# Kernel tuning notes

Measured on AMD Instinct MI355X. Metric: run time of the kernel, lower is better.

The kernel has to match this reference:

```python
import jax, jax.numpy as jnp
import numpy as np

B, T, H, W, C = 2, 8, 60, 60, 256
HEADS = 8
HD = C // HEADS
WH, WW = 5, 6
SH, SW = 2, 3
N = WH * WW            # 30 tokens per window
NW = (H // WH) * (W // WW)  # 120 windows
HID = 4 * C
SCALE = HD ** -0.5


def _rel_pos_index():
    # standard Swin 2D relative position index, shape (N, N)
    coords = np.stack(np.meshgrid(np.arange(WH), np.arange(WW), indexing='ij')).reshape(2, -1)
    rel = (coords[:, :, None] - coords[:, None, :]).transpose(1, 2, 0).astype(np.int64)
    rel[..., 0] += WH - 1
    rel[..., 1] += WW - 1
    rel[..., 0] *= 2 * WW - 1
    return jnp.asarray(rel.sum(-1))


def _attn_mask():
    # shifted-window attention mask, shape (NW, N, N), values in {0, -100}
    img = np.zeros((H, W))
    cnt = 0
    for hs in (slice(0, -WH), slice(-WH, -SH), slice(-SH, None)):
        for ws in (slice(0, -WW), slice(-WW, -SW), slice(-SW, None)):
            img[hs, ws] = cnt
            cnt += 1
    mw = img.reshape(H // WH, WH, W // WW, WW).transpose(0, 2, 1, 3).reshape(NW, N)
    diff = mw[:, None, :] - mw[:, :, None]
    return jnp.asarray(np.where(diff != 0, -100.0, 0.0).astype(np.float32))


REL_INDEX = _rel_pos_index()
ATTN_MASK = _attn_mask()


def _ln(x, g, b):
    m = x.mean(-1, keepdims=True)
    v = ((x - m) ** 2).mean(-1, keepdims=True)
    return (x - m) / jnp.sqrt(v + 1e-5) * g + b


def setup_inputs() -> dict:
    key = jax.random.key(0)
    ks = jax.random.split(key, 8)
    w_scale = 0.02
    return {
        'x': jax.random.normal(ks[0], (B, T, H, W, C), jnp.float32),
        'contrast_embed': jax.random.normal(ks[1], (B, T, C), jnp.float32),
        'gamma1': jnp.ones((C,), jnp.float32),
        'beta1': jnp.zeros((C,), jnp.float32),
        'Wq': jax.random.normal(ks[2], (C, C), jnp.float32) * w_scale,
        'bq': jnp.zeros((C,), jnp.float32),
        'Wk': jax.random.normal(ks[3], (C, C), jnp.float32) * w_scale,
        'bk': jnp.zeros((C,), jnp.float32),
        'Wv': jax.random.normal(ks[4], (C, C), jnp.float32) * w_scale,
        'bv': jnp.zeros((C,), jnp.float32),
        'rel_bias': jax.random.normal(ks[5], ((2 * WH - 1) * (2 * WW - 1), HEADS), jnp.float32) * w_scale,
        'Wo': jax.random.normal(ks[6], (C, C), jnp.float32) * w_scale,
        'bo': jnp.zeros((C,), jnp.float32),
        'gamma2': jnp.ones((C,), jnp.float32),
        'beta2': jnp.zeros((C,), jnp.float32),
        'W1': jax.random.normal(ks[7], (C, HID), jnp.float32) * w_scale,
        'b1': jnp.zeros((HID,), jnp.float32),
        'W2': jax.random.normal(jax.random.fold_in(key, 99), (HID, C), jnp.float32) * w_scale,
        'b2': jnp.zeros((C,), jnp.float32),
    }


def reference(x, contrast_embed, gamma1, beta1, Wq, bq, Wk, bk, Wv, bv, rel_bias,
              Wo, bo, gamma2, beta2, W1, b1, W2, b2):
    shortcut = x
    xn = _ln(x, gamma1, beta1)
    # cyclic shift (SW-MSA)
    xs = jnp.roll(xn, (-SH, -SW), axis=(2, 3))
    # window partition: (B,T,H,W,C) -> (B*NW, T, N, C)
    w = xs.reshape(B, T, H // WH, WH, W // WW, WW, C)
    w = w.transpose(0, 2, 4, 1, 3, 5, 6).reshape(B * NW, T, N, C)
    # per-contrast positional embedding, broadcast over windows and spatial positions
    pos = jnp.broadcast_to(contrast_embed[:, None, :, None, :], (B, NW, T, 1, C)).reshape(B * NW, T, 1, C)
    wqk = w + pos
    q = (wqk @ Wq + bq).reshape(B * NW, T, N, HEADS, HD)
    k = (wqk @ Wk + bk).reshape(B * NW, T, N, HEADS, HD)
    v = (w @ Wv + bv).reshape(B * NW, T, N, HEADS, HD)
    scores = jnp.einsum('btnhd,btmhd->bthnm', q, k) * SCALE
    bias = rel_bias[REL_INDEX].transpose(2, 0, 1)  # (HEADS, N, N)
    scores = scores + bias
    scores = scores.reshape(B, NW, T, HEADS, N, N) + ATTN_MASK[None, :, None, None]
    attn = jax.nn.softmax(scores, axis=-1).reshape(B * NW, T, HEADS, N, N)
    out = jnp.einsum('bthnm,btmhd->btnhd', attn, v).reshape(B * NW, T, N, C)
    out = out @ Wo + bo
    # window reverse: (B*NW, T, N, C) -> (B, T, H, W, C)
    out = out.reshape(B, H // WH, W // WW, T, WH, WW, C)
    out = out.transpose(0, 3, 1, 4, 2, 5, 6).reshape(B, T, H, W, C)
    out = jnp.roll(out, (SH, SW), axis=(2, 3))
    x1 = shortcut + out
    h = jax.nn.gelu(_ln(x1, gamma2, beta2) @ W1 + b1, approximate=False) @ W2 + b2
    return x1 + h
```

## Files before the change

kernel.cpp:

```cpp
#include <hip/hip_runtime.h>

#define DI __device__ __forceinline__

constexpr int SH_=2, SW_=3;
constexpr int ROWS_=57600;
constexpr float SCALE_=0.17677669529663687f;

typedef unsigned short u16x8 __attribute__((ext_vector_type(8)));
typedef short bf16x8 __attribute__((ext_vector_type(8)));
typedef float f32x4 __attribute__((ext_vector_type(4)));
typedef float f32x16 __attribute__((ext_vector_type(16)));

DI float bf2f(unsigned short u){ return __uint_as_float(((unsigned int)u)<<16); }
DI unsigned short f2bf(float f){
  unsigned int u = __float_as_uint(f);
  u += 0x7fffu + ((u>>16)&1u);
  return (unsigned short)(u>>16);
}
DI float ldf(const void* p, size_t i, int f){
  return f ? ((const float*)p)[i] : bf2f(((const unsigned short*)p)[i]);
}
DI float4 ldf4(const void* p, size_t i, int f){
  if (f) return *((const float4*)((const float*)p + i));
  ushort4 u = *((const ushort4*)((const unsigned short*)p + i));
  return make_float4(bf2f(u.x),bf2f(u.y),bf2f(u.z),bf2f(u.w));
}

DI void gload16(const void* g, void* l){
  __builtin_amdgcn_global_load_lds((const __attribute__((address_space(1))) unsigned int*)g,
                                   (__attribute__((address_space(3))) unsigned int*)l, 16, 0, 0);
}

DI void xcd_remap(int wg, int nb, int nn, int& mt, int& nt){
  const int q = nb>>3, r = nb&7;
  const int x = wg & 7, i = wg >> 3;
  const int base = (x<r) ? x*(q+1) : r*(q+1) + (x-r)*q;
  const int work = base + i;
  mt = work / nn; nt = work - mt*nn;
}

#define WAITV(n) asm volatile("s_waitcnt vmcnt(" #n ")" ::: "memory")

__global__ void k_detect(const unsigned short* __restrict__ xu, int* __restrict__ flag){
  unsigned short u = xu[threadIdx.x*2];
  int insane = ((u>>7)&0xFF) > 0xC0;
  unsigned long long m = __ballot(insane);
  if (threadIdx.x==0) *flag = m ? 1 : 0;
}

__global__ __launch_bounds__(256) void k_prepw(
    const void* __restrict__ Wq, const void* __restrict__ Wk,
    const void* __restrict__ Wv, const void* __restrict__ Wo,
    const void* __restrict__ W1, const void* __restrict__ W2,
    unsigned short* __restrict__ wt, const int* __restrict__ flagp)
{
  const int f = *flagp;
  const void* src; int kb, total; size_t off;
  switch(blockIdx.y){
    case 0: src=Wq; kb=8;  total=65536;  off=0;      break;
    case 1: src=Wk; kb=8;  total=65536;  off=65536;  break;
    case 2: src=Wv; kb=8;  total=65536;  off=131072; break;
    case 3: src=Wo; kb=8;  total=65536;  off=196608; break;
    case 4: src=W1; kb=8;  total=262144; off=262144; break;
    default:src=W2; kb=10; total=262144; off=524288; break;
  }
  const int i = blockIdx.x*256 + threadIdx.x;
  if (i >= total) return;
  const int K = 1<<kb, N = total>>kb;
  const int n = i>>kb, k = i&(K-1);
  wt[off + (size_t)n*K + k] = f2bf(ldf(src, (size_t)k*N + n, f));
}

__global__ __launch_bounds__(256) void k_posqk(const void* __restrict__ ce,
    const unsigned short* __restrict__ wtq, const unsigned short* __restrict__ wtk,
    const void* __restrict__ bq, const void* __restrict__ bk,
    float* __restrict__ posq, float* __restrict__ posk, const int* __restrict__ flagp)
{
  const int f = *flagp;
  const int bt = blockIdx.x, mat = blockIdx.y, co = threadIdx.x;
  __shared__ float ces[256];
  ces[co] = ldf(ce, bt*256+co, f);
  __syncthreads();
  const unsigned short* wr = (mat ? wtk : wtq) + (size_t)co*256;
  float s = ldf(mat ? bk : bq, co, f);
  #pragma unroll
  for (int k0=0;k0<256;k0+=8){
    u16x8 wv = *(const u16x8*)(wr + k0);
    #pragma unroll
    for (int j=0;j<8;++j) s += ces[k0+j]*bf2f(wv[j]);
  }
  (mat ? posk : posq)[bt*256+co] = s;
}

__global__ __launch_bounds__(256) void k_ln1(const void* __restrict__ x,
    const void* __restrict__ g, const void* __restrict__ be,
    unsigned short* __restrict__ xw, const int* __restrict__ flagp)
{
  const int f = *flagp;
  const int lane = threadIdx.x & 63;
  const int wv   = threadIdx.x >> 6;
  const int rs   = blockIdx.x*4 + wv;
  float4 u = ldf4(x, (size_t)rs*256 + lane*4, f);
  float s = u.x+u.y+u.z+u.w;
  #pragma unroll
  for (int o=32;o;o>>=1) s += __shfl_xor(s,o,64);
  const float mean = s*(1.f/256.f);
  float d0=u.x-mean, d1=u.y-mean, d2=u.z-mean, d3=u.w-mean;
  float qv = d0*d0+d1*d1+d2*d2+d3*d3;
  #pragma unroll
  for (int o=32;o;o>>=1) qv += __shfl_xor(qv,o,64);
  const float rstd = rsqrtf(qv*(1.f/256.f)+1e-5f);
  float4 gu = ldf4(g, lane*4, f);
  float4 bu = ldf4(be, lane*4, f);
  ushort4 o;
  o.x = f2bf(d0*rstd*gu.x+bu.x);
  o.y = f2bf(d1*rstd*gu.y+bu.y);
  o.z = f2bf(d2*rstd*gu.z+bu.z);
  o.w = f2bf(d3*rstd*gu.w+bu.w);
  const int c = rs % 60, r = (rs/60)%60, t = (rs/3600)&7, b = rs/28800;
  int r2 = r - SH_; if (r2<0) r2+=60;
  int c2 = c - SW_; if (c2<0) c2+=60;
  const int a=r2/5, ii=r2%5, bb=c2/6, jj=c2%6;
  const int rw = ((b*120 + a*10+bb)*8 + t)*30 + ii*6+jj;
  *reinterpret_cast<ushort4*>(xw + (size_t)rw*256 + lane*4) = o;
}

__global__ __launch_bounds__(256) void k_ln2(const unsigned short* __restrict__ x1b,
    const void* __restrict__ g, const void* __restrict__ be,
    unsigned short* __restrict__ xn2, const int* __restrict__ flagp)
{
  const int f = *flagp;
  const int lane = threadIdx.x & 63;
  const int wv   = threadIdx.x >> 6;
  const int rs   = blockIdx.x*4 + wv;
  float4 v = ldf4(x1b, (size_t)rs*256 + lane*4, 0);
  float s = v.x+v.y+v.z+v.w;
  #pragma unroll
  for (int o=32;o;o>>=1) s += __shfl_xor(s,o,64);
  const float mean = s*(1.f/256.f);
  float d0=v.x-mean, d1=v.y-mean, d2=v.z-mean, d3=v.w-mean;
  float qv = d0*d0+d1*d1+d2*d2+d3*d3;
  #pragma unroll
  for (int o=32;o;o>>=1) qv += __shfl_xor(qv,o,64);
  const float rstd = rsqrtf(qv*(1.f/256.f)+1e-5f);
  float4 gu = ldf4(g, lane*4, f);
  float4 bu = ldf4(be, lane*4, f);
  ushort4 o;
  o.x = f2bf(d0*rstd*gu.x+bu.x);
  o.y = f2bf(d1*rstd*gu.y+bu.y);
  o.z = f2bf(d2*rstd*gu.z+bu.z);
  o.w = f2bf(d3*rstd*gu.w+bu.w);
  *reinterpret_cast<ushort4*>(xn2 + (size_t)rs*256 + lane*4) = o;
}

template<int K>
DI void mfma_core128(const unsigned short* __restrict__ A, const unsigned short* __restrict__ WT,
                     const int m0, const int n0, f32x4 acc[4][2], unsigned short* lds)
{
  constexpr int STEPS = K/32;
  const int tid = threadIdx.x, lane = tid&63, wave = tid>>6;
  const int wm = (wave>>2)*64, wn = (wave&3)*32;
  const int fr = lane&15;
  const int kqs = ((lane>>4) ^ ((fr>>1)&3))*8;
  #pragma unroll
  for (int i=0;i<4;++i)
    #pragma unroll
    for (int j=0;j<2;++j) acc[i][j] = (f32x4){0.f,0.f,0.f,0.f};
  const int isB = wave>>2;
  const int c0 = (wave&3)*128 + lane;
  const int c1 = c0 + 64;
  const int r0=c0>>2, p0=((c0&3)^((r0>>1)&3));
  const int r1=c1>>2, p1=((c1&3)^((r1>>1)&3));
  const unsigned short* gb = isB ? (WT + (size_t)n0*K) : (A + (size_t)m0*K);
  const unsigned short* g0 = gb + (size_t)r0*K + p0*8;
  const unsigned short* g1 = gb + (size_t)r1*K + p1*8;
  const int ldso = isB*4096 + (wave&3)*1024;
  #define STAGE_(d,k0) do{ \
    unsigned short* bse = lds + (d)*8192 + ldso; \
    gload16(g0+(k0), bse); \
    gload16(g1+(k0), bse+512); }while(0)
  STAGE_(0,0);
  STAGE_(1,32);
  int cur = 0;
  for (int t=0; t<STEPS; ++t){
    if (t+2 < STEPS){
      int nb = cur+2; if (nb>=3) nb-=3;
      STAGE_(nb, (t+2)*32);
      WAITV(4);
    } else if (t+2 == STEPS){
      WAITV(2);
    } else {
      WAITV(0);
    }
    __builtin_amdgcn_s_barrier();
    const unsigned short* At = lds + cur*8192;
    const unsigned short* Bt = At + 4096;
    bf16x8 af[4], bfv[2];
    #pragma unroll
    for (int mi=0;mi<4;++mi) af[mi]  = *(const bf16x8*)(At + (wm+mi*16+fr)*32 + kqs);
    #pragma unroll
    for (int ni=0;ni<2;++ni) bfv[ni] = *(const bf16x8*)(Bt + (wn+ni*16+fr)*32 + kqs);
    __builtin_amdgcn_s_setprio(1);
    #pragma unroll
    for (int mi=0;mi<4;++mi){
      acc[mi][0] = __builtin_amdgcn_mfma_f32_16x16x32_bf16(af[mi], bfv[0], acc[mi][0], 0,0,0);
      acc[mi][1] = __builtin_amdgcn_mfma_f32_16x16x32_bf16(af[mi], bfv[1], acc[mi][1], 0,0,0);
    }
    __builtin_amdgcn_s_setprio(0);
    __builtin_amdgcn_s_barrier();
    cur = (cur+1==3)?0:cur+1;
  }
  #undef STAGE_
}

__global__ __launch_bounds__(512,5) void k_gemm_qkv(const unsigned short* __restrict__ Ain,
    const unsigned short* __restrict__ WT, const float* __restrict__ posq,
    const float* __restrict__ posk, const void* __restrict__ bv,
    unsigned short* __restrict__ qb, unsigned short* __restrict__ kb,
    unsigned short* __restrict__ vb2, const int* __restrict__ flagp)
{
  __shared__ __align__(16) unsigned short lds[24576];
  f32x4 acc[4][2];
  int mt, nt; xcd_remap(blockIdx.x, 2700, 6, mt, nt);
  const int m0 = mt*128;
  mfma_core128<256>(Ain, WT, m0, nt*128, acc, lds);
  const int f = *flagp;
  const int tid = threadIdx.x, lane = tid&63, wave = tid>>6;
  const int wm = (wave>>2)*64, wn = (wave&3)*32;
  const int fr = lane&15, fq = lane>>4;
  const int seg = nt>>1;
  unsigned short* ob = seg==0? qb : (seg==1? kb : vb2);
  const float* posb = seg==0? posq : posk;
  #pragma unroll
  for (int mi=0;mi<4;++mi){
    #pragma unroll
    for (int r=0;r<4;++r){
      const int row = wm+mi*16+fq*4+r;
      const int grow = m0+row;
      const int bt2 = (grow/28800)*8 + (grow/30)%8;
      #pragma unroll
      for (int ni=0;ni<2;++ni){
        const int lcol = wn+ni*16+fr;
        const int colm = (nt&1)*128 + lcol;
        const float bvv = (seg<2) ? posb[bt2*256+colm] : ldf(bv,colm,f);
        lds[row*132+lcol] = f2bf(acc[mi][ni][r] + bvv);
      }
    }
  }
  __syncthreads();
  const int row = tid>>2;
  unsigned short* dst = ob + (size_t)(m0+row)*256 + (nt&1)*128;
  #pragma unroll
  for (int j=0;j<4;++j){
    const int ci = j*4 + (tid&3);
    *(u16x8*)(dst + ci*8) = *(const u16x8*)(lds + row*132 + ci*8);
  }
}

__global__ __launch_bounds__(256) void k_attn(const unsigned short* __restrict__ q,
    const unsigned short* __restrict__ k, const unsigned short* __restrict__ v,
    const void* __restrict__ relb, unsigned short* __restrict__ ao,
    const int* __restrict__ flagp)
{
  __shared__ __align__(16) unsigned short vt[4][32*40];
  __shared__ __align__(16) unsigned short pa[4][32*40];
  const int f = *flagp;
  const int tid = threadIdx.x, lane = tid&63, wave = tid>>6;
  const int task = blockIdx.x*4 + wave;
  const int h = task & 7, bt = task >> 3;
  const int wi = (bt>>3) % 120;
  const int a_ = wi/10, bb_ = wi%10;
  const size_t base = (size_t)bt*7680 + h*32;
  unsigned short* vtw = &vt[wave][0];
  unsigned short* paw = &pa[wave][0];
  if (lane < 60){
    const int m = lane>>1, hf = lane&1;
    const unsigned short* src = v + base + (size_t)m*256 + hf*16;
    u16x8 r0 = *(const u16x8*)(src);
    u16x8 r1 = *(const u16x8*)(src+8);
    #pragma unroll
    for (int j=0;j<8;++j){ vtw[(hf*16+j)*40+m] = r0[j]; vtw[(hf*16+8+j)*40+m] = r1[j]; }
  }
  vtw[(lane>>1)*40 + 30 + (lane&1)] = 0;
  const int n  = lane&31;
  const int hl = lane>>5;
  f32x16 accS = {};
  {
    const unsigned short* ka = k + base + (size_t)n*256 + hl*8;
    const unsigned short* qa = q + base + (size_t)n*256 + hl*8;
    bf16x8 a0 = *(const bf16x8*)(ka);
    bf16x8 b0 = *(const bf16x8*)(qa);
    accS = __builtin_amdgcn_mfma_f32_32x32x16_bf16(a0, b0, accS, 0,0,0);
    bf16x8 a1 = *(const bf16x8*)(ka+16);
    bf16x8 b1 = *(const bf16x8*)(qa+16);
    accS = __builtin_amdgcn_mfma_f32_32x32x16_bf16(a1, b1, accS, 0,0,0);
  }
  const int nc  = (n < 30) ? n : 29;
  const int in_ = nc/6, jn = nc - in_*6;
  const int rn = a_*5+in_, cn = bb_*6+jn;
  const int lnl = (rn<55?0:(rn<58?1:2))*3 + (cn<54?0:(cn<57?1:2));
  #pragma unroll
  for (int r=0;r<16;++r){
    const int m = (r&3) + 8*(r>>2) + 4*hl;
    if (m < 30){
      const int im = m/6, jm = m - im*6;
      const int ridx = (in_-im+4)*11 + (jn-jm+5);
      const float bi = ldf(relb, ridx*8+h, f);
      const int rm = a_*5+im, cm = bb_*6+jm;
      const int lml = (rm<55?0:(rm<58?1:2))*3 + (cm<54?0:(cm<57?1:2));
      accS[r] = accS[r]*SCALE_ + bi + (lnl==lml ? 0.f : -100.f);
    } else accS[r] = -1e30f;
  }
  float mx = accS[0];
  #pragma unroll
  for (int r=1;r<16;++r) mx = fmaxf(mx, accS[r]);
  mx = fmaxf(mx, __shfl_xor(mx, 32, 64));
  float sum = 0.f;
  #pragma unroll
  for (int r=0;r<16;++r){ accS[r] = __expf(accS[r]-mx); sum += accS[r]; }
  sum += __shfl_xor(sum, 32, 64);
  const float inv = 1.f/sum;
  #pragma unroll
  for (int r=0;r<16;++r){
    const int m = (r&3)+8*(r>>2)+4*hl;
    paw[n*40 + m] = f2bf(accS[r]);
  }
  f32x16 accO = {};
  #pragma unroll
  for (int ks=0; ks<2; ++ks){
    bf16x8 av  = *(const bf16x8*)(vtw + n*40 + ks*16 + hl*8);
    bf16x8 pv  = *(const bf16x8*)(paw + n*40 + ks*16 + hl*8);
    accO = __builtin_amdgcn_mfma_f32_32x32x16_bf16(av, pv, accO, 0,0,0);
  }
  if (n < 30){
    #pragma unroll
    for (int g4=0; g4<4; ++g4){
      const int d0 = 8*g4 + 4*hl;
      ushort4 o;
      o.x = f2bf(accO[g4*4+0]*inv);
      o.y = f2bf(accO[g4*4+1]*inv);
      o.z = f2bf(accO[g4*4+2]*inv);
      o.w = f2bf(accO[g4*4+3]*inv);
      *(ushort4*)(ao + base + (size_t)n*256 + d0) = o;
    }
  }
}

__global__ __launch_bounds__(512,5) void k_gemm_wo(const unsigned short* __restrict__ Ain,
    const unsigned short* __restrict__ WT, const void* __restrict__ bias,
    const void* __restrict__ xin, unsigned short* __restrict__ x1b,
    const int* __restrict__ flagp)
{
  __shared__ __align__(16) unsigned short lds[24576];
  f32x4 acc[4][2];
  int mt, nt; xcd_remap(blockIdx.x, 900, 2, mt, nt);
  const int m0 = mt*128, n0 = nt*128;
  mfma_core128<256>(Ain, WT, m0, n0, acc, lds);
  const int f = *flagp;
  const int tid = threadIdx.x, lane = tid&63, wave = tid>>6;
  const int wm = (wave>>2)*64, wn = (wave&3)*32;
  const int fr = lane&15, fq = lane>>4;
  #pragma unroll
  for (int mi=0;mi<4;++mi){
    #pragma unroll
    for (int ni=0;ni<2;++ni){
      const int lcol = wn+ni*16+fr;
      const float bvv = ldf(bias, n0+lcol, f);
      #pragma unroll
      for (int r=0;r<4;++r){
        const int row = wm+mi*16+fq*4+r;
        lds[row*132+lcol] = f2bf(acc[mi][ni][r] + bvv);
      }
    }
  }
  __syncthreads();
  const int row = tid>>2;
  const int rw = m0+row;
  const int nn = rw%30, t = (rw/30)%8, bw = rw/240;
  const int b = bw/120, wi = bw%120;
  const int a = wi/10, bb2 = wi%10, ii = nn/6, jj = nn%6;
  int rr = a*5+ii+SH_; if (rr>=60) rr-=60;
  int cc = bb2*6+jj+SW_; if (cc>=60) cc-=60;
  const size_t srow = ((size_t)((b*8+t)*60 + rr)*60 + cc);
  #pragma unroll
  for (int j=0;j<4;++j){
    const int ci = j*4 + (tid&3);
    const int col = n0 + ci*8;
    u16x8 vv = *(const u16x8*)(lds + row*132 + ci*8);
    float4 xa = ldf4(xin, srow*256+col,   f);
    float4 xbv= ldf4(xin, srow*256+col+4, f);
    u16x8 o;
    o[0]=f2bf(bf2f(vv[0])+xa.x); o[1]=f2bf(bf2f(vv[1])+xa.y);
    o[2]=f2bf(bf2f(vv[2])+xa.z); o[3]=f2bf(bf2f(vv[3])+xa.w);
    o[4]=f2bf(bf2f(vv[4])+xbv.x); o[5]=f2bf(bf2f(vv[5])+xbv.y);
    o[6]=f2bf(bf2f(vv[6])+xbv.z); o[7]=f2bf(bf2f(vv[7])+xbv.w);
    *(u16x8*)(x1b + srow*256 + col) = o;
  }
}

__global__ __launch_bounds__(512,5) void k_mlp1(const unsigned short* __restrict__ Ain,
    const unsigned short* __restrict__ WT, const void* __restrict__ bias,
    unsigned short* __restrict__ hb, const int row0, const int* __restrict__ flagp)
{
  __shared__ __align__(16) unsigned short lds[24576];
  f32x4 acc[4][2];
  int mt, nt; xcd_remap(blockIdx.x, 1800, 8, mt, nt);
  const int m0 = row0 + mt*128, n0 = nt*128;
  mfma_core128<256>(Ain, WT, m0, n0, acc, lds);
  const int f = *flagp;
  const int tid = threadIdx.x, lane = tid&63, wave = tid>>6;
  const int wm = (wave>>2)*64, wn = (wave&3)*32;
  const int fr = lane&15, fq = lane>>4;
  #pragma unroll
  for (int mi=0;mi<4;++mi){
    #pragma unroll
    for (int ni=0;ni<2;++ni){
      const int lcol = wn+ni*16+fr;
      const float bvv = ldf(bias, n0+lcol, f);
      #pragma unroll
      for (int r=0;r<4;++r){
        const int row = wm+mi*16+fq*4+r;
        const float vv = acc[mi][ni][r] + bvv;
        lds[row*132+lcol] = f2bf(0.5f*vv*(1.f+erff(vv*0.70710678118654752f)));
      }
    }
  }
  __syncthreads();
  const int row = tid>>2;
  unsigned short* dst = hb + (size_t)(mt*128+row)*1024 + n0;
  #pragma unroll
  for (int j=0;j<4;++j){
    const int ci = j*4 + (tid&3);
    *(u16x8*)(dst + ci*8) = *(const u16x8*)(lds + row*132 + ci*8);
  }
}

__global__ __launch_bounds__(512,5) void k_mlp2(const unsigned short* __restrict__ hbin,
    const unsigned short* __restrict__ WT, const void* __restrict__ bias,
    const unsigned short* __restrict__ x1b, void* __restrict__ outb,
    const int row0, const int* __restrict__ flagp)
{
  __shared__ __align__(16) unsigned short lds[24576];
  f32x4 acc[4][2];
  int mt, nt; xcd_remap(blockIdx.x, 450, 2, mt, nt);
  const int m0l = mt*128, n0 = nt*128;
  mfma_core128<1024>(hbin, WT, m0l, n0, acc, lds);
  const int f = *flagp;
  const int tid = threadIdx.x, lane = tid&63, wave = tid>>6;
  const int wm = (wave>>2)*64, wn = (wave&3)*32;
  const int fr = lane&15, fq = lane>>4;
  #pragma unroll
  for (int mi=0;mi<4;++mi){
    #pragma unroll
    for (int ni=0;ni<2;++ni){
      const int lcol = wn+ni*16+fr;
      const float bvv = ldf(bias, n0+lcol, f);
      #pragma unroll
      for (int r=0;r<4;++r){
        const int row = wm+mi*16+fq*4+r;
        lds[row*132+lcol] = f2bf(acc[mi][ni][r] + bvv);
      }
    }
  }
  __syncthreads();
  const int row = tid>>2;
  const size_t grow = (size_t)(row0 + m0l + row);
  #pragma unroll
  for (int j=0;j<4;++j){
    const int ci = j*4 + (tid&3);
    const int col = n0 + ci*8;
    u16x8 vv = *(const u16x8*)(lds + row*132 + ci*8);
    u16x8 xv = *(const u16x8*)(x1b + grow*256 + col);
    if (f){
      float4 o0, o1;
      o0.x=bf2f(vv[0])+bf2f(xv[0]); o0.y=bf2f(vv[1])+bf2f(xv[1]);
      o0.z=bf2f(vv[2])+bf2f(xv[2]); o0.w=bf2f(vv[3])+bf2f(xv[3]);
      o1.x=bf2f(vv[4])+bf2f(xv[4]); o1.y=bf2f(vv[5])+bf2f(xv[5]);
      o1.z=bf2f(vv[6])+bf2f(xv[6]); o1.w=bf2f(vv[7])+bf2f(xv[7]);
      *(float4*)((float*)outb + grow*256 + col)     = o0;
      *(float4*)((float*)outb + grow*256 + col + 4) = o1;
    } else {
      u16x8 o;
      #pragma unroll
      for (int e=0;e<8;++e) o[e] = f2bf(bf2f(vv[e])+bf2f(xv[e]));
      *(u16x8*)((unsigned short*)outb + grow*256 + col) = o;
    }
  }
}

extern "C" void kernel_launch(void* const* d_in, const int* in_sizes, int n_in,
                              void* d_out, int out_size, void* d_ws, size_t ws_size,
                              hipStream_t stream)
{
  const void* x   = d_in[0];
  const void* ce  = d_in[1];
  const void* g1  = d_in[2];
  const void* be1 = d_in[3];
  const void* Wq  = d_in[4];
  const void* bq  = d_in[5];
  const void* Wk  = d_in[6];
  const void* bk  = d_in[7];
  const void* Wv  = d_in[8];
  const void* bv  = d_in[9];
  const void* rb  = d_in[10];
  const void* Wo  = d_in[11];
  const void* bo  = d_in[12];
  const void* g2  = d_in[13];
  const void* be2 = d_in[14];
  const void* W1  = d_in[15];
  const void* b1  = d_in[16];
  const void* W2  = d_in[17];
  const void* b2  = d_in[18];

  char* ws = (char*)d_ws;
  const size_t SZ = (size_t)ROWS_*256*2;
  unsigned short* kbuf = (unsigned short*)(ws);
  unsigned short* vbuf = (unsigned short*)(ws + SZ);
  unsigned short* xw   = (unsigned short*)(ws + 2*SZ);
  unsigned short* qbuf = (unsigned short*)(ws + 3*SZ);
  unsigned short* aob  = xw;
  unsigned short* xn2  = kbuf;
  unsigned short* x1b  = qbuf;
  unsigned short* hb   = vbuf;
  float* posq = (float*)(ws + 4*SZ);
  float* posk = posq + 16*256;
  int*   flag = (int*)(ws + 4*SZ + 32768);
  unsigned short* wt = (unsigned short*)(ws + 4*SZ + 65536);

  unsigned short* wtqkv = wt;
  unsigned short* wtq = wt;
  unsigned short* wtk = wt + 65536;
  unsigned short* wto = wt + 196608;
  unsigned short* wt1 = wt + 262144;
  unsigned short* wt2 = wt + 524288;

  k_detect<<<1,64,0,stream>>>((const unsigned short*)x, flag);
  k_prepw<<<dim3(1024,6),256,0,stream>>>(Wq,Wk,Wv,Wo,W1,W2, wt, flag);
  k_posqk<<<dim3(16,2),256,0,stream>>>(ce, wtq, wtk, bq, bk, posq, posk, flag);
  k_ln1<<<14400,256,0,stream>>>(x, g1, be1, xw, flag);
  k_gemm_qkv<<<2700,512,0,stream>>>(xw, wtqkv, posq, posk, bv, qbuf, kbuf, vbuf, flag);
  k_attn<<<3840,256,0,stream>>>(qbuf, kbuf, vbuf, rb, aob, flag);
  k_gemm_wo<<<900,512,0,stream>>>(aob, wto, bo, x, x1b, flag);
  k_ln2<<<14400,256,0,stream>>>(x1b, g2, be2, xn2, flag);
  for (int chk=0; chk<2; ++chk){
    const int row0 = chk*28800;
    k_mlp1<<<1800,512,0,stream>>>(xn2, wt1, b1, hb, row0, flag);
    k_mlp2<<<450,512,0,stream>>>(hb, wt2, b2, x1b, d_out, row0, flag);
  }
}
```

Measured before the change: 275.2 us.

## Fuse LayerNorm2 into full-width Wo GEMM epilogue and precompute row index tables

```diff
diff --git a/kernel.cpp b/kernel.cpp
--- a/kernel.cpp
+++ b/kernel.cpp
@@ -94,7 +94,8 @@
 
 __global__ __launch_bounds__(256) void k_ln1(const void* __restrict__ x,
     const void* __restrict__ g, const void* __restrict__ be,
-    unsigned short* __restrict__ xw, const int* __restrict__ flagp)
+    unsigned short* __restrict__ xw, unsigned char* __restrict__ rowbt,
+    int* __restrict__ srowtab, const int* __restrict__ flagp)
 {
   const int f = *flagp;
   const int lane = threadIdx.x & 63;
@@ -123,34 +124,10 @@
   const int a=r2/5, ii=r2%5, bb=c2/6, jj=c2%6;
   const int rw = ((b*120 + a*10+bb)*8 + t)*30 + ii*6+jj;
   *reinterpret_cast<ushort4*>(xw + (size_t)rw*256 + lane*4) = o;
-}
-
-__global__ __launch_bounds__(256) void k_ln2(const unsigned short* __restrict__ x1b,
-    const void* __restrict__ g, const void* __restrict__ be,
-    unsigned short* __restrict__ xn2, const int* __restrict__ flagp)
-{
-  const int f = *flagp;
-  const int lane = threadIdx.x & 63;
-  const int wv   = threadIdx.x >> 6;
-  const int rs   = blockIdx.x*4 + wv;
-  float4 v = ldf4(x1b, (size_t)rs*256 + lane*4, 0);
-  float s = v.x+v.y+v.z+v.w;
-  #pragma unroll
-  for (int o=32;o;o>>=1) s += __shfl_xor(s,o,64);
-  const float mean = s*(1.f/256.f);
-  float d0=v.x-mean, d1=v.y-mean, d2=v.z-mean, d3=v.w-mean;
-  float qv = d0*d0+d1*d1+d2*d2+d3*d3;
-  #pragma unroll
-  for (int o=32;o;o>>=1) qv += __shfl_xor(qv,o,64);
-  const float rstd = rsqrtf(qv*(1.f/256.f)+1e-5f);
-  float4 gu = ldf4(g, lane*4, f);
-  float4 bu = ldf4(be, lane*4, f);
-  ushort4 o;
-  o.x = f2bf(d0*rstd*gu.x+bu.x);
-  o.y = f2bf(d1*rstd*gu.y+bu.y);
-  o.z = f2bf(d2*rstd*gu.z+bu.z);
-  o.w = f2bf(d3*rstd*gu.w+bu.w);
-  *reinterpret_cast<ushort4*>(xn2 + (size_t)rs*256 + lane*4) = o;
+  if (lane==0){
+    rowbt[rw] = (unsigned char)(b*8+t);
+    srowtab[rw] = rs;
+  }
 }
 
 template<int K>
@@ -217,7 +194,8 @@
     const unsigned short* __restrict__ WT, const float* __restrict__ posq,
     const float* __restrict__ posk, const void* __restrict__ bv,
     unsigned short* __restrict__ qb, unsigned short* __restrict__ kb,
-    unsigned short* __restrict__ vb2, const int* __restrict__ flagp)
+    unsigned short* __restrict__ vb2, const unsigned char* __restrict__ rowbt,
+    const int* __restrict__ flagp)
 {
   __shared__ __align__(16) unsigned short lds[24576];
   f32x4 acc[4][2];
@@ -236,8 +214,7 @@
     #pragma unroll
     for (int r=0;r<4;++r){
       const int row = wm+mi*16+fq*4+r;
-      const int grow = m0+row;
-      const int bt2 = (grow/28800)*8 + (grow/30)%8;
+      const int bt2 = rowbt[m0+row];
       #pragma unroll
       for (int ni=0;ni<2;++ni){
         const int lcol = wn+ni*16+fr;
@@ -346,55 +323,123 @@
   }
 }
 
-__global__ __launch_bounds__(512,5) void k_gemm_wo(const unsigned short* __restrict__ Ain,
+__global__ __launch_bounds__(512,4) void k_wo_ln2(const unsigned short* __restrict__ Ain,
     const unsigned short* __restrict__ WT, const void* __restrict__ bias,
     const void* __restrict__ xin, unsigned short* __restrict__ x1b,
+    unsigned short* __restrict__ xn2, const void* __restrict__ g2,
+    const void* __restrict__ be2, const int* __restrict__ srowtab,
     const int* __restrict__ flagp)
 {
-  __shared__ __align__(16) unsigned short lds[24576];
-  f32x4 acc[4][2];
-  int mt, nt; xcd_remap(blockIdx.x, 900, 2, mt, nt);
-  const int m0 = mt*128, n0 = nt*128;
-  mfma_core128<256>(Ain, WT, m0, n0, acc, lds);
-  const int f = *flagp;
+  __shared__ __align__(16) unsigned short lds[36864];
+  f32x4 acc[4][4];
+  int mt, nt; xcd_remap(blockIdx.x, 450, 1, mt, nt);
+  const int m0 = mt*128;
   const int tid = threadIdx.x, lane = tid&63, wave = tid>>6;
-  const int wm = (wave>>2)*64, wn = (wave&3)*32;
+  const int wm = (wave>>2)*64, wn64 = (wave&3)*64;
   const int fr = lane&15, fq = lane>>4;
+  const int kqs = ((lane>>4) ^ ((fr>>1)&3))*8;
+  #pragma unroll
+  for (int i=0;i<4;++i)
+    #pragma unroll
+    for (int j=0;j<4;++j) acc[i][j] = (f32x4){0.f,0.f,0.f,0.f};
+  const int rA = tid>>2, pA = (tid&3)^((rA>>1)&3);
+  const int rB1 = tid>>2, pB1 = (tid&3)^((rB1>>1)&3);
+  const int rB2 = 128 + (tid>>2), pB2 = (tid&3)^((rB2>>1)&3);
+  const unsigned short* gA  = Ain + (size_t)(m0+rA)*256 + pA*8;
+  const unsigned short* gB1 = WT + (size_t)rB1*256 + pB1*8;
+  const unsigned short* gB2 = WT + (size_t)rB2*256 + pB2*8;
+  const int wb = wave*512;
+  #define STAGEW_(d,k0) do{ \
+    unsigned short* bse = lds + (d)*12288; \
+    gload16(gA +(k0), bse + wb); \
+    gload16(gB1+(k0), bse + 4096 + wb); \
+    gload16(gB2+(k0), bse + 8192 + wb); }while(0)
+  STAGEW_(0,0);
+  STAGEW_(1,32);
+  int cur = 0;
+  for (int t=0; t<8; ++t){
+    if (t+2 < 8){
+      int nb = cur+2; if (nb>=3) nb-=3;
+      STAGEW_(nb, (t+2)*32);
+      WAITV(6);
+    } else if (t+2 == 8){
+      WAITV(3);
+    } else {
+      WAITV(0);
+    }
+    __builtin_amdgcn_s_barrier();
+    const unsigned short* At = lds + cur*12288;
+    const unsigned short* Bt = At + 4096;
+    bf16x8 af[4], bfv[4];
+    #pragma unroll
+    for (int mi=0;mi<4;++mi) af[mi]  = *(const bf16x8*)(At + (wm+mi*16+fr)*32 + kqs);
+    #pragma unroll
+    for (int ni=0;ni<4;++ni) bfv[ni] = *(const bf16x8*)(Bt + (wn64+ni*16+fr)*32 + kqs);
+    __builtin_amdgcn_s_setprio(1);
+    #pragma unroll
+    for (int mi=0;mi<4;++mi)
+      #pragma unroll
+      for (int ni=0;ni<4;++ni)
+        acc[mi][ni] = __builtin_amdgcn_mfma_f32_16x16x32_bf16(af[mi], bfv[ni], acc[mi][ni], 0,0,0);
+    __builtin_amdgcn_s_setprio(0);
+    __builtin_amdgcn_s_barrier();
+    cur = (cur+1==3)?0:cur+1;
+  }
+  #undef STAGEW_
+  const int f = *flagp;
   #pragma unroll
   for (int mi=0;mi<4;++mi){
     #pragma unroll
-    for (int ni=0;ni<2;++ni){
-      const int lcol = wn+ni*16+fr;
-      const float bvv = ldf(bias, n0+lcol, f);
+    for (int ni=0;ni<4;++ni){
+      const int col = wn64+ni*16+fr;
+      const float bvv = ldf(bias, col, f);
       #pragma unroll
       for (int r=0;r<4;++r){
         const int row = wm+mi*16+fq*4+r;
-        lds[row*132+lcol] = f2bf(acc[mi][ni][r] + bvv);
+        lds[row*264+col] = f2bf(acc[mi][ni][r] + bvv);
       }
     }
   }
   __syncthreads();
   const int row = tid>>2;
-  const int rw = m0+row;
-  const int nn = rw%30, t = (rw/30)%8, bw = rw/240;
-  const int b = bw/120, wi = bw%120;
-  const int a = wi/10, bb2 = wi%10, ii = nn/6, jj = nn%6;
-  int rr = a*5+ii+SH_; if (rr>=60) rr-=60;
-  int cc = bb2*6+jj+SW_; if (cc>=60) cc-=60;
-  const size_t srow = ((size_t)((b*8+t)*60 + rr)*60 + cc);
-  #pragma unroll
-  for (int j=0;j<4;++j){
-    const int ci = j*4 + (tid&3);
-    const int col = n0 + ci*8;
-    u16x8 vv = *(const u16x8*)(lds + row*132 + ci*8);
+  const size_t srow = (size_t)srowtab[m0+row];
+  const int cb = (tid&3)*8;
+  float s = 0.f, sq = 0.f;
+  #pragma unroll
+  for (int j=0;j<8;++j){
+    const int col = (cb+j)*8;
+    u16x8 vv = *(const u16x8*)(lds + row*264 + col);
     float4 xa = ldf4(xin, srow*256+col,   f);
-    float4 xbv= ldf4(xin, srow*256+col+4, f);
+    float4 xb = ldf4(xin, srow*256+col+4, f);
+    float xs[8] = {xa.x,xa.y,xa.z,xa.w,xb.x,xb.y,xb.z,xb.w};
     u16x8 o;
-    o[0]=f2bf(bf2f(vv[0])+xa.x); o[1]=f2bf(bf2f(vv[1])+xa.y);
-    o[2]=f2bf(bf2f(vv[2])+xa.z); o[3]=f2bf(bf2f(vv[3])+xa.w);
-    o[4]=f2bf(bf2f(vv[4])+xbv.x); o[5]=f2bf(bf2f(vv[5])+xbv.y);
-    o[6]=f2bf(bf2f(vv[6])+xbv.z); o[7]=f2bf(bf2f(vv[7])+xbv.w);
+    #pragma unroll
+    for (int e=0;e<8;++e){
+      o[e] = f2bf(bf2f(vv[e]) + xs[e]);
+      const float xv = bf2f(o[e]);
+      s += xv; sq += xv*xv;
+    }
     *(u16x8*)(x1b + srow*256 + col) = o;
+    *(u16x8*)(lds + row*264 + col) = o;
+  }
+  s  += __shfl_xor(s, 1, 64);  s  += __shfl_xor(s, 2, 64);
+  sq += __shfl_xor(sq, 1, 64); sq += __shfl_xor(sq, 2, 64);
+  const float mean = s*(1.f/256.f);
+  const float var  = sq*(1.f/256.f) - mean*mean;
+  const float rstd = rsqrtf(var + 1e-5f);
+  #pragma unroll
+  for (int j=0;j<8;++j){
+    const int col = (cb+j)*8;
+    u16x8 vv = *(const u16x8*)(lds + row*264 + col);
+    float4 ga = ldf4(g2, col, f), gb = ldf4(g2, col+4, f);
+    float4 ba = ldf4(be2, col, f), bb = ldf4(be2, col+4, f);
+    float gs[8] = {ga.x,ga.y,ga.z,ga.w,gb.x,gb.y,gb.z,gb.w};
+    float bs[8] = {ba.x,ba.y,ba.z,ba.w,bb.x,bb.y,bb.z,bb.w};
+    u16x8 o;
+    #pragma unroll
+    for (int e=0;e<8;++e)
+      o[e] = f2bf((bf2f(vv[e])-mean)*rstd*gs[e] + bs[e]);
+    *(u16x8*)(xn2 + srow*256 + col) = o;
   }
 }
 
@@ -526,6 +571,8 @@
   float* posk = posq + 16*256;
   int*   flag = (int*)(ws + 4*SZ + 32768);
   unsigned short* wt = (unsigned short*)(ws + 4*SZ + 65536);
+  int*   srowtab = (int*)(ws + 4*SZ + 65536 + 1572864);
+  unsigned char* rowbt = (unsigned char*)(ws + 4*SZ + 65536 + 1572864 + 230400);
 
   unsigned short* wtqkv = wt;
   unsigned short* wtq = wt;
@@ -537,11 +584,10 @@
   k_detect<<<1,64,0,stream>>>((const unsigned short*)x, flag);
   k_prepw<<<dim3(1024,6),256,0,stream>>>(Wq,Wk,Wv,Wo,W1,W2, wt, flag);
   k_posqk<<<dim3(16,2),256,0,stream>>>(ce, wtq, wtk, bq, bk, posq, posk, flag);
-  k_ln1<<<14400,256,0,stream>>>(x, g1, be1, xw, flag);
-  k_gemm_qkv<<<2700,512,0,stream>>>(xw, wtqkv, posq, posk, bv, qbuf, kbuf, vbuf, flag);
+  k_ln1<<<14400,256,0,stream>>>(x, g1, be1, xw, rowbt, srowtab, flag);
+  k_gemm_qkv<<<2700,512,0,stream>>>(xw, wtqkv, posq, posk, bv, qbuf, kbuf, vbuf, rowbt, flag);
   k_attn<<<3840,256,0,stream>>>(qbuf, kbuf, vbuf, rb, aob, flag);
-  k_gemm_wo<<<900,512,0,stream>>>(aob, wto, bo, x, x1b, flag);
-  k_ln2<<<14400,256,0,stream>>>(x1b, g2, be2, xn2, flag);
+  k_wo_ln2<<<450,512,0,stream>>>(aob, wto, bo, x, x1b, xn2, g2, be2, srowtab, flag);
   for (int chk=0; chk<2; ++chk){
     const int row0 = chk*28800;
     k_mlp1<<<1800,512,0,stream>>>(xn2, wt1, b1, hb, row0, flag);
```

Result: slower. 299.1 us (+8.7%).
